# Kernel tuning notes

Measured on AMD Instinct MI355X. Metric: run time of the kernel, lower is better.

Reference implementation:

```python
import jax, jax.numpy as jnp
import numpy as np

NUM_HEADS = 16


def setup_inputs() -> dict:
    key = jax.random.key(0)
    ks = jax.random.split(key, 8)
    B, L, Hd = 2, 2048, 1024
    s = 0.02
    return {
        "x": jax.random.normal(ks[0], (B, L, Hd), jnp.float32),
        "y": jax.random.normal(ks[1], (B, L, Hd), jnp.float32),
        "mask": jnp.zeros((B, L), jnp.bool_),  # True = padding (masked out)
        "Wq_w": jax.random.normal(ks[2], (Hd, Hd), jnp.float32) * s,
        "Wq_b": jnp.zeros((Hd,), jnp.float32),
        "Wkv_w": jax.random.normal(ks[3], (Hd, 2 * Hd), jnp.float32) * s,
        "Wkv_b": jnp.zeros((2 * Hd,), jnp.float32),
        "proj_w": jax.random.normal(ks[4], (Hd, Hd), jnp.float32) * s,
        "proj_b": jnp.zeros((Hd,), jnp.float32),
    }


def reference(x, y, mask, Wq_w, Wq_b, Wkv_w, Wkv_b, proj_w, proj_b):
    B, L, Hd = x.shape
    H = NUM_HEADS
    D = Hd // H
    scale = 1.0 / np.sqrt(D)

    # projections (torch Linear: stored here already as (in, out))
    q = (x @ Wq_w + Wq_b).reshape(B, L, H, D).transpose(0, 2, 1, 3)   # bhld
    kv = (y @ Wkv_w + Wkv_b).reshape(B, L, 2, H, D)
    k = kv[:, :, 0].transpose(0, 2, 1, 3)                             # bhkd
    v = kv[:, :, 1].transpose(0, 2, 1, 3)                             # bhkd

    attn = jnp.einsum("bhld,bhkd->bhlk", q, k) * scale

    # combined padding (over keys) + causal mask; True = masked
    causal = jnp.triu(jnp.ones((L, L), jnp.bool_), 1)                 # (L, L)
    combined = mask[:, None, None, :] | causal[None, None]            # (B,1,L,L)
    attn = jnp.where(combined, -jnp.inf, attn)

    p = jax.nn.softmax(attn, axis=-1)
    out = jnp.einsum("bhlk,bhkd->bhld", p, v)
    out = out.transpose(0, 2, 1, 3).reshape(B, L, Hd)
    return out @ proj_w + proj_b
```

## Files before the change

### kernel.cpp

```cpp
#include <hip/hip_runtime.h>
#include <stdint.h>

#define B_  2
#define L_  2048
#define HD_ 1024
#define H_  16
#define D_  64

typedef unsigned short u16;
typedef __attribute__((ext_vector_type(8))) short bf16x8;
typedef __attribute__((ext_vector_type(4))) float f32x4;

#define MFMA16(a, b, c) __builtin_amdgcn_mfma_f32_16x16x32_bf16((a), (b), (c), 0, 0, 0)

__device__ __forceinline__ void gload16(const void* g, void* l) {
  __builtin_amdgcn_global_load_lds((const __attribute__((address_space(1))) void*)g,
                                   (__attribute__((address_space(3))) void*)l, 16, 0, 0);
}

__device__ __forceinline__ u16 f2bf(float f) {
  union { float f; uint32_t u; } c; c.f = f;
  uint32_t u = c.u + 0x7FFFu + ((c.u >> 16) & 1u);
  return (u16)(u >> 16);
}

__device__ __forceinline__ float bf2f(u16 v) {
  union { uint32_t u; float f; } c; c.u = (uint32_t)v << 16;
  return c.f;
}

__device__ __forceinline__ uint32_t cvt_pk_bf16(float lo, float hi) {
  uint32_t r;
  asm("v_cvt_pk_bf16_f32 %0, %1, %2" : "=v"(r) : "v"(lo), "v"(hi));
  return r;
}

__global__ void prologue_k(const float* __restrict__ x, const float* __restrict__ y,
                           u16* __restrict__ xb, u16* __restrict__ yb,
                           const float* __restrict__ Wq, const float* __restrict__ Wkv,
                           const float* __restrict__ Wp,
                           u16* __restrict__ Wqt, u16* __restrict__ Wkvt,
                           u16* __restrict__ Wpt) {
  int bid = blockIdx.x;
  int t = threadIdx.x;
  if (bid < 4096) {
    const float* in = bid < 2048 ? x : y;
    u16* out = bid < 2048 ? xb : yb;
    int i = ((bid & 2047) * 256 + t) * 8;
    float4 a = *(const float4*)(in + i);
    float4 b = *(const float4*)(in + i + 4);
    bf16x8 r;
    r[0] = (short)f2bf(a.x); r[1] = (short)f2bf(a.y); r[2] = (short)f2bf(a.z); r[3] = (short)f2bf(a.w);
    r[4] = (short)f2bf(b.x); r[5] = (short)f2bf(b.y); r[6] = (short)f2bf(b.z); r[7] = (short)f2bf(b.w);
    *(bf16x8*)(out + i) = r;
    return;
  }
  int f = bid - 4096;
  const float* src; u16* dst; int Nfull, bx, by;
  if (f < 1024)      { src = Wq;  dst = Wqt;  Nfull = 1024; bx = f & 31;  by = f >> 5; }
  else if (f < 3072) { int g2 = f - 1024; src = Wkv; dst = Wkvt; Nfull = 2048; bx = g2 & 63; by = g2 >> 6; }
  else               { int g2 = f - 3072; src = Wp;  dst = Wpt;  Nfull = 1024; bx = g2 & 31; by = g2 >> 5; }
  __shared__ float tile[32][33];
  int tc = t & 31, tr = t >> 5;
  int nb = bx * 32, kb = by * 32;
#pragma unroll
  for (int i = 0; i < 4; i++)
    tile[tr + i * 8][tc] = src[(size_t)(kb + tr + i * 8) * Nfull + nb + tc];
  __syncthreads();
#pragma unroll
  for (int i = 0; i < 4; i++) {
    int nl = tr + i * 8;
    dst[(size_t)(nb + nl) * 1024 + kb + tc] = f2bf(tile[tc][nl]);
  }
}

__device__ __forceinline__ void gemm_body(
    char* sA, char* sB,
    const u16* __restrict__ A, const u16* __restrict__ Bt,
    const float* __restrict__ bias, void* __restrict__ outp,
    int N, int epi, int bm, int bn)
{
  int t = threadIdx.x;
  int lane = t & 63, w = t >> 6;
  int g = lane >> 4, l15 = lane & 15;
  int wr = w >> 1, wc = w & 1;

  f32x4 zero = {0.f, 0.f, 0.f, 0.f};
  f32x4 acc[4][4];
#pragma unroll
  for (int mi = 0; mi < 4; mi++)
#pragma unroll
    for (int ni = 0; ni < 4; ni++) acc[mi][ni] = zero;

#define GSTAGE(bufi, k0s) do {                                                          \
    _Pragma("unroll")                                                                   \
    for (int it = 0; it < 4; it++) {                                                    \
      int c = it * 256 + t;                          \
      int r = c >> 3, sp = c & 7;                                                       \
      int off = (sp ^ (r & 7)) << 4;               \
      gload16((const char*)(A + (size_t)(bm + r) * 1024 + (k0s)) + off,                 \
              sA + (bufi) * 16384 + c * 16);                                            \
      gload16((const char*)(Bt + (size_t)(bn + r) * 1024 + (k0s)) + off,                \
              sB + (bufi) * 16384 + c * 16);                                            \
    } } while (0)

  GSTAGE(0, 0);
  int buf = 0;
#pragma unroll 1
  for (int kt = 0; kt < 16; kt++) {
    __builtin_amdgcn_sched_barrier(0);
    __builtin_amdgcn_s_barrier();
    if (kt < 15) {
      GSTAGE(buf ^ 1, (kt + 1) << 6);
      asm volatile("s_waitcnt vmcnt(8)" ::: "memory");
    } else {
      asm volatile("s_waitcnt vmcnt(0)" ::: "memory");
    }
    __builtin_amdgcn_s_barrier();
    __builtin_amdgcn_sched_barrier(0);

    const char* cA = sA + buf * 16384;
    const char* cB = sB + buf * 16384;
#pragma unroll
    for (int kc = 0; kc < 2; kc++) {
      bf16x8 af[4], bfr[4];
#pragma unroll
      for (int mi = 0; mi < 4; mi++) {
        int r = wr * 64 + mi * 16 + l15;
        af[mi] = *(const bf16x8*)(cA + r * 128 + (((kc * 4 + g) ^ (r & 7)) << 4));
      }
#pragma unroll
      for (int ni = 0; ni < 4; ni++) {
        int r = wc * 64 + ni * 16 + l15;
        bfr[ni] = *(const bf16x8*)(cB + r * 128 + (((kc * 4 + g) ^ (r & 7)) << 4));
      }
#pragma unroll
      for (int mi = 0; mi < 4; mi++)
#pragma unroll
        for (int ni = 0; ni < 4; ni++)
          acc[mi][ni] = MFMA16(af[mi], bfr[ni], acc[mi][ni]);
    }
    buf ^= 1;
  }
#undef GSTAGE

  float bv[4];
#pragma unroll
  for (int ni = 0; ni < 4; ni++) bv[ni] = bias[bn + wc * 64 + ni * 16 + l15];

  if (epi == 2) {
    float* fo = (float*)outp;
#pragma unroll
    for (int mi = 0; mi < 4; mi++)
#pragma unroll
      for (int ni = 0; ni < 4; ni++) {
        int n = bn + wc * 64 + ni * 16 + l15;
#pragma unroll
        for (int r = 0; r < 4; r++) {
          int m = bm + wr * 64 + mi * 16 + g * 4 + r;
          fo[(size_t)m * N + n] = acc[mi][ni][r] + bv[ni];
        }
      }
  } else {
    const float QS = (epi == 0) ? 0.125f * 1.44269504089f : 1.0f;
    u16* ob = (u16*)outp;
#pragma unroll
    for (int mi = 0; mi < 4; mi++)
#pragma unroll
      for (int ni = 0; ni < 4; ni++) {
        int n = bn + wc * 64 + ni * 16 + l15;
        int kv = n >> 10;
        int hh = (n >> 6) & 15;
        int dd = n & 63;
        int m0 = bm + wr * 64 + mi * 16 + g * 4;
        int bb = m0 >> 11, lq0 = m0 & 2047;
        if (epi == 1 && kv == 1) {
          ushort4 pk;
          pk.x = f2bf(acc[mi][ni][0] + bv[ni]);
          pk.y = f2bf(acc[mi][ni][1] + bv[ni]);
          pk.z = f2bf(acc[mi][ni][2] + bv[ni]);
          pk.w = f2bf(acc[mi][ni][3] + bv[ni]);
          size_t idx = (size_t)(B_ * H_ * L_ * D_) +
                       (((size_t)(bb * H_ + hh) * D_ + dd) * L_ + lq0);
          *(ushort4*)(ob + idx) = pk;
        } else {
#pragma unroll
          for (int r = 0; r < 4; r++) {
            size_t idx = (((size_t)(bb * H_ + hh) * L_ + lq0 + r) * D_) + dd;
            ob[idx] = f2bf((acc[mi][ni][r] + bv[ni]) * QS);
          }
        }
      }
  }
}

__global__ __launch_bounds__(256) void qkv_k(
    const u16* __restrict__ xb, const u16* __restrict__ yb,
    const u16* __restrict__ Wqt, const u16* __restrict__ Wkvt,
    const float* __restrict__ Wq_b, const float* __restrict__ Wkv_b,
    u16* __restrict__ Qout, u16* __restrict__ KVout)
{
  __shared__ char sA[2 * 16384];
  __shared__ char sB[2 * 16384];
  int bx = blockIdx.x, by = blockIdx.y;
  if (by < 16) {
    gemm_body(sA, sB, yb, Wkvt, Wkv_b, (void*)KVout, 2048, 1, by * 128, bx * 128);
    __syncthreads();
    gemm_body(sA, sB, yb, Wkvt, Wkv_b, (void*)KVout, 2048, 1, (by + 16) * 128, bx * 128);
  } else {
    gemm_body(sA, sB, xb, Wqt, Wq_b, (void*)Qout, 1024, 0,
              (2 * (by - 16) + (bx >> 3)) * 128, (bx & 7) * 128);
  }
}

__global__ __launch_bounds__(256) void gemm_k(
    const u16* __restrict__ A, const u16* __restrict__ Bt,
    const float* __restrict__ bias, void* __restrict__ outp, int N)
{
  __shared__ char sA[2 * 16384];
  __shared__ char sB[2 * 16384];
  gemm_body(sA, sB, A, Bt, bias, outp, N, 2, blockIdx.y * 128, blockIdx.x * 128);
}

__global__ __launch_bounds__(512, 2) void attn_k(
    const u16* __restrict__ Qb, const u16* __restrict__ Kb, const u16* __restrict__ Vt,
    const unsigned char* __restrict__ pad, u16* __restrict__ Ob,
    u16* __restrict__ Opart, float* __restrict__ mlbuf)
{
  __shared__ char sK[3][8192];
  __shared__ char sV[3][8192];
  __shared__ char sP[8][2048];
  int t = threadIdx.x, lane = t & 63, w = t >> 6, g = lane >> 4, l15 = lane & 15;
  int x = blockIdx.x, h = blockIdx.y, b = blockIdx.z, bh = b * H_ + h;
  int role = x >> 3, xp = x & 7;
  int qbH = 15 - xp, qbL = xp;
  int nktH = 2 * qbH + 2;
  const int SPLIT = 17;

  const u16* Kbh = Kb + (size_t)bh * L_ * D_;
  const u16* Vbh = Vt + (size_t)bh * D_ * L_;
  const unsigned char* pdb = pad + b * L_;
  int psw = l15 & 7;

  int srr = t >> 3, ssp = t & 7;
  int sso = (ssp ^ (srr & 7)) << 4;
#define STAGE(bufi, kt0s) do {                                                        \
    gload16((const char*)(Kbh + (size_t)((kt0s) + srr) * D_) + sso, sK[bufi] + t * 16); \
    gload16((const char*)(Vbh + (size_t)srr * L_ + (kt0s)) + sso, sV[bufi] + t * 16);   \
  } while (0)

  int nphase = role ? 1 : 2;
#pragma unroll 1
  for (int ph = 0; ph < nphase; ph++) {
    int qb, lo, hi, mode;
    if (role) { qb = qbH; lo = 0;     hi = SPLIT;     mode = 1; }
    else if (ph == 0) { qb = qbL; lo = 0; hi = 2 * qbL + 2; mode = 0; }
    else { qb = qbH; lo = SPLIT; hi = nktH; mode = 2; }

    int qw0 = qb * 128 + w * 16;
    int bound = qw0 + 15;

    const u16* qp = Qb + ((size_t)bh * L_ + qw0 + l15) * D_ + g * 8;
    bf16x8 qf0 = *(const bf16x8*)qp;
    bf16x8 qf1 = *(const bf16x8*)(qp + 32);

    f32x4 zero = {0.f, 0.f, 0.f, 0.f};
    f32x4 oacc[4];
#pragma unroll
    for (int db = 0; db < 4; db++) oacc[db] = zero;
    float mrun = -1e30f, lrun = 0.f;

    if (ph) __syncthreads();
    STAGE(0, lo << 6);
    int cb = 0, nb = 1;

#pragma unroll 1
    for (int kt = lo; kt < hi; kt++) {
      int kt0 = kt << 6;
      __builtin_amdgcn_sched_barrier(0);
      if (kt + 1 < hi) {
        STAGE(nb, (kt + 1) << 6);
        asm volatile("s_waitcnt vmcnt(2)" ::: "memory");
      } else {
        asm volatile("s_waitcnt vmcnt(0)" ::: "memory");
      }
      __builtin_amdgcn_s_barrier();
      __builtin_amdgcn_sched_barrier(0);

      if (kt0 <= bound) {
        float sc[4][4];
#pragma unroll
        for (int s = 0; s < 4; s++) {
          int kb = kt0 + s * 16;
          bool live = (kb <= bound);
          f32x4 st = zero;
          uint32_t pb = 0;
          if (live) {
            int R = s * 16 + l15, sw = l15 & 7;
            bf16x8 kf0 = *(const bf16x8*)(sK[cb] + R * 128 + ((g ^ sw) << 4));
            bf16x8 kf1 = *(const bf16x8*)(sK[cb] + R * 128 + (((4 + g) ^ sw) << 4));
            st = MFMA16(kf0, qf0, st);
            st = MFMA16(kf1, qf1, st);
            pb = *(const uint32_t*)(pdb + kb + 4 * g);
          }
          bool needm = !live || (kb + 15 > qw0) || (__ballot(pb != 0) != 0);
          if (needm) {
#pragma unroll
            for (int r = 0; r < 4; r++) {
              int key = kb + 4 * g + r;
              bool pm = (pb >> (8 * r)) & 0xffu;
              bool msk = !live || pm || (key > qw0 + l15);
              sc[s][r] = msk ? -1e30f : st[r];
            }
          } else {
#pragma unroll
            for (int r = 0; r < 4; r++) sc[s][r] = st[r];
          }
        }

        float m0 = fmaxf(fmaxf(sc[0][0], sc[0][1]), fmaxf(sc[0][2], sc[0][3]));
        float m1 = fmaxf(fmaxf(sc[1][0], sc[1][1]), fmaxf(sc[1][2], sc[1][3]));
        float m2 = fmaxf(fmaxf(sc[2][0], sc[2][1]), fmaxf(sc[2][2], sc[2][3]));
        float m3 = fmaxf(fmaxf(sc[3][0], sc[3][1]), fmaxf(sc[3][2], sc[3][3]));
        float mt = fmaxf(fmaxf(m0, m1), fmaxf(m2, m3));
        mt = fmaxf(mt, __shfl_xor(mt, 16));
        mt = fmaxf(mt, __shfl_xor(mt, 32));
        if (!__all(mt <= mrun + 8.0f)) {
          float mnew = fmaxf(mrun, mt);
          float al = __builtin_amdgcn_exp2f(mrun - mnew);
          mrun = mnew;
          lrun *= al;
#pragma unroll
          for (int db = 0; db < 4; db++)
#pragma unroll
            for (int r = 0; r < 4; r++) oacc[db][r] *= al;
        }
        float rs = 0.f;
        char* pwb = sP[w] + l15 * 128 + (g & 1) * 8;
#pragma unroll
        for (int s = 0; s < 4; s++) {
          float p0 = __builtin_amdgcn_exp2f(sc[s][0] - mrun);
          float p1 = __builtin_amdgcn_exp2f(sc[s][1] - mrun);
          float p2 = __builtin_amdgcn_exp2f(sc[s][2] - mrun);
          float p3 = __builtin_amdgcn_exp2f(sc[s][3] - mrun);
          rs += (p0 + p1) + (p2 + p3);
          uint32_t w0 = cvt_pk_bf16(p0, p1), w1 = cvt_pk_bf16(p2, p3);
          char* dst = pwb + (((2 * s + (g >> 1)) ^ psw) << 4);
          *(uint32_t*)dst = w0;
          *(uint32_t*)(dst + 4) = w1;
        }
        rs += __shfl_xor(rs, 16);
        rs += __shfl_xor(rs, 32);
        lrun += rs;

#pragma unroll
        for (int kc = 0; kc < 2; kc++) {
          if (kt0 + 32 * kc <= bound) {
            bf16x8 pf = *(const bf16x8*)(sP[w] + l15 * 128 + (((4 * kc + g) ^ psw) << 4));
#pragma unroll
            for (int db = 0; db < 4; db++) {
              int dR = db * 16 + l15;
              bf16x8 vf = *(const bf16x8*)(sV[cb] + dR * 128 +
                                           (((4 * kc + g) ^ (dR & 7)) << 4));
              oacc[db] = MFMA16(vf, pf, oacc[db]);
            }
          }
        }
      }
      cb = (cb == 2) ? 0 : cb + 1;
      nb = (nb == 2) ? 0 : nb + 1;
    }

    float rl = (lrun != 0.f) ? 1.0f / lrun : 0.f;
    int q = qw0 + l15;
    if (mode == 0) {
      u16* op = Ob + ((size_t)b * L_ + q) * HD_ + h * D_ + g * 4;
#pragma unroll
      for (int db = 0; db < 4; db++) {
        ushort4 pk;
        pk.x = f2bf(oacc[db][0] * rl);
        pk.y = f2bf(oacc[db][1] * rl);
        pk.z = f2bf(oacc[db][2] * rl);
        pk.w = f2bf(oacc[db][3] * rl);
        *(ushort4*)(op + db * 16) = pk;
      }
    } else {
      int part = mode - 1;
      size_t prow = (size_t)part * 32768 + (size_t)bh * 1024 + (q - 1024);
      u16* op = Opart + prow * 64 + g * 4;
#pragma unroll
      for (int db = 0; db < 4; db++) {
        ushort4 pk;
        pk.x = f2bf(oacc[db][0] * rl);
        pk.y = f2bf(oacc[db][1] * rl);
        pk.z = f2bf(oacc[db][2] * rl);
        pk.w = f2bf(oacc[db][3] * rl);
        *(ushort4*)(op + db * 16) = pk;
      }
      if (g == 0) {
        mlbuf[prow * 2]     = mrun;
        mlbuf[prow * 2 + 1] = lrun;
      }
    }
  }
#undef STAGE
}

__global__ __launch_bounds__(256) void merge_k(
    const u16* __restrict__ Op, const float* __restrict__ ml, u16* __restrict__ Ob)
{
  int tid = blockIdx.x * 256 + threadIdx.x;
  int d0 = (tid & 7) * 8;
  int row = tid >> 3;
  int qrel = row & 1023, bh = row >> 10;
  int b = bh >> 4, h = bh & 15;
  float m0 = ml[(size_t)row * 2],            l0 = ml[(size_t)row * 2 + 1];
  float m1 = ml[((size_t)32768 + row) * 2],  l1 = ml[((size_t)32768 + row) * 2 + 1];
  float M = fmaxf(m0, m1);
  float w0 = l0 * __builtin_amdgcn_exp2f(m0 - M);
  float w1 = l1 * __builtin_amdgcn_exp2f(m1 - M);
  float rw = 1.0f / (w0 + w1);
  w0 *= rw; w1 *= rw;
  bf16x8 a = *(const bf16x8*)(Op + (size_t)row * 64 + d0);
  bf16x8 c = *(const bf16x8*)(Op + ((size_t)32768 + row) * 64 + d0);
  bf16x8 o;
#pragma unroll
  for (int j = 0; j < 8; j++)
    o[j] = (short)f2bf(w0 * bf2f((u16)a[j]) + w1 * bf2f((u16)c[j]));
  *(bf16x8*)(Ob + ((size_t)b * L_ + 1024 + qrel) * HD_ + h * D_ + d0) = o;
}

extern "C" void kernel_launch(void* const* d_in, const int* in_sizes, int n_in,
                              void* d_out, int out_size, void* d_ws, size_t ws_size,
                              hipStream_t stream) {
  const float* x      = (const float*)d_in[0];
  const float* y      = (const float*)d_in[1];
  const unsigned char* mask = (const unsigned char*)d_in[2];
  const float* Wq_w   = (const float*)d_in[3];
  const float* Wq_b   = (const float*)d_in[4];
  const float* Wkv_w  = (const float*)d_in[5];
  const float* Wkv_b  = (const float*)d_in[6];
  const float* proj_w = (const float*)d_in[7];
  const float* proj_b = (const float*)d_in[8];

  char* ws = (char*)d_ws;
  u16* xb   = (u16*)(ws);
  u16* yb   = (u16*)(ws + (size_t)(8  << 20));
  u16* Wqt  = (u16*)(ws + (size_t)(16 << 20));
  u16* Wkvt = (u16*)(ws + (size_t)(18 << 20));
  u16* Wpt  = (u16*)(ws + (size_t)(22 << 20));
  u16* Qb   = (u16*)(ws + (size_t)(24 << 20));
  u16* Kb   = (u16*)(ws + (size_t)(32 << 20));
  u16* Vtb  = (u16*)(ws + (size_t)(40 << 20));
  u16* Ob   = xb;
  u16* Opart  = yb;
  float* mlbuf = (float*)Wqt;

  hipLaunchKernelGGL(prologue_k, dim3(8192), dim3(256), 0, stream,
                     x, y, xb, yb, Wq_w, Wkv_w, proj_w, Wqt, Wkvt, Wpt);
  hipLaunchKernelGGL(qkv_k, dim3(16, 32), dim3(256), 0, stream,
                     xb, yb, Wqt, Wkvt, Wq_b, Wkv_b, Qb, Kb);
  hipLaunchKernelGGL(attn_k, dim3(16, H_, B_), dim3(512), 0, stream,
                     Qb, Kb, Vtb, mask, Ob, Opart, mlbuf);
  hipLaunchKernelGGL(merge_k, dim3(1024), dim3(256), 0, stream, Opart, mlbuf, Ob);
  hipLaunchKernelGGL(gemm_k, dim3(8, 32), dim3(256), 0, stream, Ob, Wpt, proj_b, d_out, 1024);
}
```

Baseline: 122.9 us.

## Use 64x128-tile output projection GEMM and hoist padding-mask check in attention

Replaces the generic 128x128 output-projection GEMM with a dedicated 64x128-tile kernel, doubling the grid to 512 blocks so more CUs are busy on the 4096x1024 output. Separately, the attention kernel now scans the whole padding row once at startup and skips the per-tile padding loads and ballots when no key is padded. Smaller tiles lower per-block operand reuse, and the pad prescan adds a small upfront read per block.

```diff
diff --git a/kernel.cpp b/kernel.cpp
--- a/kernel.cpp
+++ b/kernel.cpp
@@ -213,13 +213,97 @@
   }
 }
 
-__global__ __launch_bounds__(256) void gemm_k(
+__global__ __launch_bounds__(256) void proj_k(
     const u16* __restrict__ A, const u16* __restrict__ Bt,
-    const float* __restrict__ bias, void* __restrict__ outp, int N)
+    const float* __restrict__ bias, float* __restrict__ fo)
 {
-  __shared__ char sA[2 * 16384];
+  __shared__ char sA[2 * 8192];
   __shared__ char sB[2 * 16384];
-  gemm_body(sA, sB, A, Bt, bias, outp, N, 2, blockIdx.y * 128, blockIdx.x * 128);
+  int t = threadIdx.x;
+  int lane = t & 63, w = t >> 6;
+  int g = lane >> 4, l15 = lane & 15;
+  int wr = w >> 1, wc = w & 1;
+  int bm = blockIdx.y * 64, bn = blockIdx.x * 128;
+
+  f32x4 zero = {0.f, 0.f, 0.f, 0.f};
+  f32x4 acc[2][4];
+#pragma unroll
+  for (int mi = 0; mi < 2; mi++)
+#pragma unroll
+    for (int ni = 0; ni < 4; ni++) acc[mi][ni] = zero;
+
+#define PSTAGE(bufi, k0s) do {                                                          \
+    _Pragma("unroll")                                                                   \
+    for (int it = 0; it < 2; it++) {             \
+      int c = it * 256 + t;                                                             \
+      int r = c >> 3, sp = c & 7;                                                       \
+      int off = (sp ^ (r & 7)) << 4;                                                    \
+      gload16((const char*)(A + (size_t)(bm + r) * 1024 + (k0s)) + off,                 \
+              sA + (bufi) * 8192 + c * 16);                                             \
+    }                                                                                   \
+    _Pragma("unroll")                                                                   \
+    for (int it = 0; it < 4; it++) {           \
+      int c = it * 256 + t;                                                             \
+      int r = c >> 3, sp = c & 7;                                                       \
+      int off = (sp ^ (r & 7)) << 4;                                                    \
+      gload16((const char*)(Bt + (size_t)(bn + r) * 1024 + (k0s)) + off,                \
+              sB + (bufi) * 16384 + c * 16);                                            \
+    } } while (0)
+
+  PSTAGE(0, 0);
+  int buf = 0;
+#pragma unroll 1
+  for (int kt = 0; kt < 16; kt++) {
+    __builtin_amdgcn_sched_barrier(0);
+    __builtin_amdgcn_s_barrier();
+    if (kt < 15) {
+      PSTAGE(buf ^ 1, (kt + 1) << 6);
+      asm volatile("s_waitcnt vmcnt(6)" ::: "memory");
+    } else {
+      asm volatile("s_waitcnt vmcnt(0)" ::: "memory");
+    }
+    __builtin_amdgcn_s_barrier();
+    __builtin_amdgcn_sched_barrier(0);
+
+    const char* cA = sA + buf * 8192;
+    const char* cB = sB + buf * 16384;
+#pragma unroll
+    for (int kc = 0; kc < 2; kc++) {
+      bf16x8 af[2], bfr[4];
+#pragma unroll
+      for (int mi = 0; mi < 2; mi++) {
+        int r = wr * 32 + mi * 16 + l15;
+        af[mi] = *(const bf16x8*)(cA + r * 128 + (((kc * 4 + g) ^ (r & 7)) << 4));
+      }
+#pragma unroll
+      for (int ni = 0; ni < 4; ni++) {
+        int r = wc * 64 + ni * 16 + l15;
+        bfr[ni] = *(const bf16x8*)(cB + r * 128 + (((kc * 4 + g) ^ (r & 7)) << 4));
+      }
+#pragma unroll
+      for (int mi = 0; mi < 2; mi++)
+#pragma unroll
+        for (int ni = 0; ni < 4; ni++)
+          acc[mi][ni] = MFMA16(af[mi], bfr[ni], acc[mi][ni]);
+    }
+    buf ^= 1;
+  }
+#undef PSTAGE
+
+  float bv[4];
+#pragma unroll
+  for (int ni = 0; ni < 4; ni++) bv[ni] = bias[bn + wc * 64 + ni * 16 + l15];
+#pragma unroll
+  for (int mi = 0; mi < 2; mi++)
+#pragma unroll
+    for (int ni = 0; ni < 4; ni++) {
+      int n = bn + wc * 64 + ni * 16 + l15;
+#pragma unroll
+      for (int r = 0; r < 4; r++) {
+        int m = bm + wr * 32 + mi * 16 + g * 4 + r;
+        fo[(size_t)m * 1024 + n] = acc[mi][ni][r] + bv[ni];
+      }
+    }
 }
 
 __global__ __launch_bounds__(512, 2) void attn_k(
@@ -242,6 +326,12 @@
   const unsigned char* pdb = pad + b * L_;
   int psw = l15 & 7;
 
+  const uint4* pp = (const uint4*)pdb;
+  uint4 pv0 = pp[lane];
+  uint4 pv1 = pp[64 + lane];
+  uint32_t nzp = pv0.x | pv0.y | pv0.z | pv0.w | pv1.x | pv1.y | pv1.z | pv1.w;
+  bool anyp = __ballot(nzp != 0) != 0;
+
   int srr = t >> 3, ssp = t & 7;
   int sso = (ssp ^ (srr & 7)) << 4;
 #define STAGE(bufi, kt0s) do {                                                        \
@@ -301,9 +391,9 @@
             bf16x8 kf1 = *(const bf16x8*)(sK[cb] + R * 128 + (((4 + g) ^ sw) << 4));
             st = MFMA16(kf0, qf0, st);
             st = MFMA16(kf1, qf1, st);
-            pb = *(const uint32_t*)(pdb + kb + 4 * g);
+            if (anyp) pb = *(const uint32_t*)(pdb + kb + 4 * g);
           }
-          bool needm = !live || (kb + 15 > qw0) || (__ballot(pb != 0) != 0);
+          bool needm = !live || (kb + 15 > qw0) || anyp;
           if (needm) {
 #pragma unroll
             for (int r = 0; r < 4; r++) {
@@ -463,5 +553,5 @@
   hipLaunchKernelGGL(attn_k, dim3(16, H_, B_), dim3(512), 0, stream,
                      Qb, Kb, Vtb, mask, Ob, Opart, mlbuf);
   hipLaunchKernelGGL(merge_k, dim3(1024), dim3(256), 0, stream, Opart, mlbuf, Ob);
-  hipLaunchKernelGGL(gemm_k, dim3(8, 32), dim3(256), 0, stream, Ob, Wpt, proj_b, d_out, 1024);
-}
+  hipLaunchKernelGGL(proj_k, dim3(8, 64), dim3(256), 0, stream, Ob, Wpt, proj_b, (float*)d_out);
+}
```

Measured after the change: 116.4 us. 5.3% less time.

## Use 64x128 GEMM tiles for QKV and projection, hoist padding-mask check

Applied to the files above, without the earlier changes.

The GEMM tile shrinks from 128x128 to 64x128, which halves the A staging buffer and lets three blocks occupy each CU. The QKV launch becomes a flat 24x64 grid, replacing the earlier scheme where some blocks ran two GEMM tiles in sequence, and the projection uses more, smaller blocks, so load is spread more evenly across the 256 CUs. Separately, the attention kernel scans the whole padding row once at the start. When no key is padded it skips the per-tile mask loads and ballots. The cost is less data reuse per block, since there are more B-tile reloads per output.

```diff
diff --git a/kernel.cpp b/kernel.cpp
--- a/kernel.cpp
+++ b/kernel.cpp
@@ -74,7 +74,7 @@
   }
 }
 
-__device__ __forceinline__ void gemm_body(
+__device__ __forceinline__ void gemm64_body(
     char* sA, char* sB,
     const u16* __restrict__ A, const u16* __restrict__ Bt,
     const float* __restrict__ bias, void* __restrict__ outp,
@@ -86,47 +86,53 @@
   int wr = w >> 1, wc = w & 1;
 
   f32x4 zero = {0.f, 0.f, 0.f, 0.f};
-  f32x4 acc[4][4];
-#pragma unroll
-  for (int mi = 0; mi < 4; mi++)
+  f32x4 acc[2][4];
+#pragma unroll
+  for (int mi = 0; mi < 2; mi++)
 #pragma unroll
     for (int ni = 0; ni < 4; ni++) acc[mi][ni] = zero;
 
-#define GSTAGE(bufi, k0s) do {                                                          \
+#define GSTAGE64(bufi, k0s) do {                                                        \
     _Pragma("unroll")                                                                   \
-    for (int it = 0; it < 4; it++) {                                                    \
-      int c = it * 256 + t;                          \
+    for (int it = 0; it < 2; it++) {             \
+      int c = it * 256 + t;                                                             \
       int r = c >> 3, sp = c & 7;                                                       \
-      int off = (sp ^ (r & 7)) << 4;               \
+      int off = (sp ^ (r & 7)) << 4;                                                    \
       gload16((const char*)(A + (size_t)(bm + r) * 1024 + (k0s)) + off,                 \
-              sA + (bufi) * 16384 + c * 16);                                            \
+              sA + (bufi) * 8192 + c * 16);                                             \
+    }                                                                                   \
+    _Pragma("unroll")                                                                   \
+    for (int it = 0; it < 4; it++) {           \
+      int c = it * 256 + t;                                                             \
+      int r = c >> 3, sp = c & 7;                                                       \
+      int off = (sp ^ (r & 7)) << 4;                                                    \
       gload16((const char*)(Bt + (size_t)(bn + r) * 1024 + (k0s)) + off,                \
               sB + (bufi) * 16384 + c * 16);                                            \
     } } while (0)
 
-  GSTAGE(0, 0);
+  GSTAGE64(0, 0);
   int buf = 0;
 #pragma unroll 1
   for (int kt = 0; kt < 16; kt++) {
     __builtin_amdgcn_sched_barrier(0);
     __builtin_amdgcn_s_barrier();
     if (kt < 15) {
-      GSTAGE(buf ^ 1, (kt + 1) << 6);
-      asm volatile("s_waitcnt vmcnt(8)" ::: "memory");
+      GSTAGE64(buf ^ 1, (kt + 1) << 6);
+      asm volatile("s_waitcnt vmcnt(6)" ::: "memory");
     } else {
       asm volatile("s_waitcnt vmcnt(0)" ::: "memory");
     }
     __builtin_amdgcn_s_barrier();
     __builtin_amdgcn_sched_barrier(0);
 
-    const char* cA = sA + buf * 16384;
+    const char* cA = sA + buf * 8192;
     const char* cB = sB + buf * 16384;
 #pragma unroll
     for (int kc = 0; kc < 2; kc++) {
-      bf16x8 af[4], bfr[4];
-#pragma unroll
-      for (int mi = 0; mi < 4; mi++) {
-        int r = wr * 64 + mi * 16 + l15;
+      bf16x8 af[2], bfr[4];
+#pragma unroll
+      for (int mi = 0; mi < 2; mi++) {
+        int r = wr * 32 + mi * 16 + l15;
         af[mi] = *(const bf16x8*)(cA + r * 128 + (((kc * 4 + g) ^ (r & 7)) << 4));
       }
 #pragma unroll
@@ -135,14 +141,14 @@
         bfr[ni] = *(const bf16x8*)(cB + r * 128 + (((kc * 4 + g) ^ (r & 7)) << 4));
       }
 #pragma unroll
-      for (int mi = 0; mi < 4; mi++)
+      for (int mi = 0; mi < 2; mi++)
 #pragma unroll
         for (int ni = 0; ni < 4; ni++)
           acc[mi][ni] = MFMA16(af[mi], bfr[ni], acc[mi][ni]);
     }
     buf ^= 1;
   }
-#undef GSTAGE
+#undef GSTAGE64
 
   float bv[4];
 #pragma unroll
@@ -151,13 +157,13 @@
   if (epi == 2) {
     float* fo = (float*)outp;
 #pragma unroll
-    for (int mi = 0; mi < 4; mi++)
+    for (int mi = 0; mi < 2; mi++)
 #pragma unroll
       for (int ni = 0; ni < 4; ni++) {
         int n = bn + wc * 64 + ni * 16 + l15;
 #pragma unroll
         for (int r = 0; r < 4; r++) {
-          int m = bm + wr * 64 + mi * 16 + g * 4 + r;
+          int m = bm + wr * 32 + mi * 16 + g * 4 + r;
           fo[(size_t)m * N + n] = acc[mi][ni][r] + bv[ni];
         }
       }
@@ -165,14 +171,14 @@
     const float QS = (epi == 0) ? 0.125f * 1.44269504089f : 1.0f;
     u16* ob = (u16*)outp;
 #pragma unroll
-    for (int mi = 0; mi < 4; mi++)
+    for (int mi = 0; mi < 2; mi++)
 #pragma unroll
       for (int ni = 0; ni < 4; ni++) {
         int n = bn + wc * 64 + ni * 16 + l15;
         int kv = n >> 10;
         int hh = (n >> 6) & 15;
         int dd = n & 63;
-        int m0 = bm + wr * 64 + mi * 16 + g * 4;
+        int m0 = bm + wr * 32 + mi * 16 + g * 4;
         int bb = m0 >> 11, lq0 = m0 & 2047;
         if (epi == 1 && kv == 1) {
           ushort4 pk;
@@ -194,32 +200,29 @@
   }
 }
 
-__global__ __launch_bounds__(256) void qkv_k(
+__global__ __launch_bounds__(256, 3) void qkv_k(
     const u16* __restrict__ xb, const u16* __restrict__ yb,
     const u16* __restrict__ Wqt, const u16* __restrict__ Wkvt,
     const float* __restrict__ Wq_b, const float* __restrict__ Wkv_b,
     u16* __restrict__ Qout, u16* __restrict__ KVout)
 {
-  __shared__ char sA[2 * 16384];
+  __shared__ char sA[2 * 8192];
   __shared__ char sB[2 * 16384];
-  int bx = blockIdx.x, by = blockIdx.y;
-  if (by < 16) {
-    gemm_body(sA, sB, yb, Wkvt, Wkv_b, (void*)KVout, 2048, 1, by * 128, bx * 128);
-    __syncthreads();
-    gemm_body(sA, sB, yb, Wkvt, Wkv_b, (void*)KVout, 2048, 1, (by + 16) * 128, bx * 128);
-  } else {
-    gemm_body(sA, sB, xb, Wqt, Wq_b, (void*)Qout, 1024, 0,
-              (2 * (by - 16) + (bx >> 3)) * 128, (bx & 7) * 128);
-  }
-}
-
-__global__ __launch_bounds__(256) void gemm_k(
+  int bx = blockIdx.x, bm = blockIdx.y * 64;
+  if (bx < 16)
+    gemm64_body(sA, sB, yb, Wkvt, Wkv_b, (void*)KVout, 2048, 1, bm, bx * 128);
+  else
+    gemm64_body(sA, sB, xb, Wqt, Wq_b, (void*)Qout, 1024, 0, bm, (bx - 16) * 128);
+}
+
+__global__ __launch_bounds__(256, 3) void proj_k(
     const u16* __restrict__ A, const u16* __restrict__ Bt,
-    const float* __restrict__ bias, void* __restrict__ outp, int N)
+    const float* __restrict__ bias, float* __restrict__ fo)
 {
-  __shared__ char sA[2 * 16384];
+  __shared__ char sA[2 * 8192];
   __shared__ char sB[2 * 16384];
-  gemm_body(sA, sB, A, Bt, bias, outp, N, 2, blockIdx.y * 128, blockIdx.x * 128);
+  gemm64_body(sA, sB, A, Bt, bias, (void*)fo, 1024, 2,
+              blockIdx.y * 64, blockIdx.x * 128);
 }
 
 __global__ __launch_bounds__(512, 2) void attn_k(
@@ -242,6 +245,12 @@
   const unsigned char* pdb = pad + b * L_;
   int psw = l15 & 7;
 
+  const uint4* pp = (const uint4*)pdb;
+  uint4 pv0 = pp[lane];
+  uint4 pv1 = pp[64 + lane];
+  uint32_t nzp = pv0.x | pv0.y | pv0.z | pv0.w | pv1.x | pv1.y | pv1.z | pv1.w;
+  bool anyp = __ballot(nzp != 0) != 0;
+
   int srr = t >> 3, ssp = t & 7;
   int sso = (ssp ^ (srr & 7)) << 4;
 #define STAGE(bufi, kt0s) do {                                                        \
@@ -301,9 +310,9 @@
             bf16x8 kf1 = *(const bf16x8*)(sK[cb] + R * 128 + (((4 + g) ^ sw) << 4));
             st = MFMA16(kf0, qf0, st);
             st = MFMA16(kf1, qf1, st);
-            pb = *(const uint32_t*)(pdb + kb + 4 * g);
+            if (anyp) pb = *(const uint32_t*)(pdb + kb + 4 * g);
           }
-          bool needm = !live || (kb + 15 > qw0) || (__ballot(pb != 0) != 0);
+          bool needm = !live || (kb + 15 > qw0) || anyp;
           if (needm) {
 #pragma unroll
             for (int r = 0; r < 4; r++) {
@@ -458,10 +467,10 @@
 
   hipLaunchKernelGGL(prologue_k, dim3(8192), dim3(256), 0, stream,
                      x, y, xb, yb, Wq_w, Wkv_w, proj_w, Wqt, Wkvt, Wpt);
-  hipLaunchKernelGGL(qkv_k, dim3(16, 32), dim3(256), 0, stream,
+  hipLaunchKernelGGL(qkv_k, dim3(24, 64), dim3(256), 0, stream,
                      xb, yb, Wqt, Wkvt, Wq_b, Wkv_b, Qb, Kb);
   hipLaunchKernelGGL(attn_k, dim3(16, H_, B_), dim3(512), 0, stream,
                      Qb, Kb, Vtb, mask, Ob, Opart, mlbuf);
   hipLaunchKernelGGL(merge_k, dim3(1024), dim3(256), 0, stream, Opart, mlbuf, Ob);
-  hipLaunchKernelGGL(gemm_k, dim3(8, 32), dim3(256), 0, stream, Ob, Wpt, proj_b, d_out, 1024);
-}
+  hipLaunchKernelGGL(proj_k, dim3(8, 64), dim3(256), 0, stream, Ob, Wpt, proj_b, (float*)d_out);
+}
```

After: 114.6 us. 6.8% less time.
